# Kernel optimization log

Measured on AMD Instinct MI355X. Metric: run time of the kernel, lower is better.

## Reference

```python
import jax, jax.numpy as jnp
import numpy as np

EMBED_DIM = 1024
NUM_HEADS = 16
SCALE = (EMBED_DIM // NUM_HEADS) ** -0.5  # 0.125


def setup_inputs() -> dict:
    key = jax.random.key(0)
    ks = jax.random.split(key, 9)
    B, S, E = 4, 2048, EMBED_DIM
    std = E ** -0.5
    x = jax.random.normal(ks[0], (B, S, E), dtype=jnp.float32)
    Wq = jax.random.normal(ks[1], (E, E), dtype=jnp.float32) * std
    bq = jax.random.normal(ks[2], (E,), dtype=jnp.float32) * 0.01
    Wk = jax.random.normal(ks[3], (E, E), dtype=jnp.float32) * std
    bk = jax.random.normal(ks[4], (E,), dtype=jnp.float32) * 0.01
    Wv = jax.random.normal(ks[5], (E, E), dtype=jnp.float32) * std
    bv = jax.random.normal(ks[6], (E,), dtype=jnp.float32) * 0.01
    Wo = jax.random.normal(ks[7], (E, E), dtype=jnp.float32) * std
    bo = jax.random.normal(ks[8], (E,), dtype=jnp.float32) * 0.01
    return {"x": x, "Wq": Wq, "bq": bq, "Wk": Wk, "bk": bk,
            "Wv": Wv, "bv": bv, "Wo": Wo, "bo": bo}


def reference(x, Wq, bq, Wk, bk, Wv, bv, Wo, bo):
    # torch nn.Linear: y = x @ W.T + b
    q = jnp.einsum('bse,fe->bsf', x, Wq) + bq   # [B,S,E]
    k = jnp.einsum('bse,fe->bsf', x, Wk) + bk
    v = jnp.einsum('bse,fe->bsf', x, Wv) + bv
    # Bilinear (no softmax) attention: scores = (Q K^T) * scale
    scores = jnp.einsum('bse,bte->bst', q, k) * SCALE  # [B,S,S]
    out = jnp.einsum('bst,bte->bse', scores, v)        # [B,S,E]
    return jnp.einsum('bse,fe->bsf', out, Wo) + bo
```

## Files before the change

kernel.cpp:

```cpp
#include <hip/hip_runtime.h>
#include <stdint.h>

typedef __bf16 bf16_t;
typedef __bf16 bf16x8 __attribute__((ext_vector_type(8)));
typedef __bf16 bf16x4 __attribute__((ext_vector_type(4)));
typedef float floatx4 __attribute__((ext_vector_type(4)));

__device__ __forceinline__ void async_copy16(const bf16_t* g, bf16_t* l) {
  __builtin_amdgcn_global_load_lds(
      (const __attribute__((address_space(1))) void*)g,
      (__attribute__((address_space(3))) void*)l, 16, 0, 0);
}

struct CvtSeg { const float* s; bf16_t* d; long n; };
struct CvtArgs { CvtSeg seg[5]; };

__global__ void cvt_multi(CvtArgs a) {
  CvtSeg sg = a.seg[blockIdx.y];
#pragma unroll
  for (int it = 0; it < 4; it++) {
    long i = (((long)blockIdx.x + (long)it * 2048) * 256 + threadIdx.x) * 4;
    if (i < sg.n) {
      float4 f = *(const float4*)(sg.s + i);
      bf16x4 o;
      o[0] = (bf16_t)f.x; o[1] = (bf16_t)f.y; o[2] = (bf16_t)f.z; o[3] = (bf16_t)f.w;
      *(bf16x4*)(sg.d + i) = o;
    }
  }
}

__global__ __launch_bounds__(256, 2) void qkv3(
    const bf16_t* __restrict__ xb,
    const bf16_t* __restrict__ Wq, const bf16_t* __restrict__ Wk, const bf16_t* __restrict__ Wv,
    const float* __restrict__ bq, const float* __restrict__ bk, const float* __restrict__ bv,
    bf16_t* __restrict__ qout, bf16_t* __restrict__ kT, bf16_t* __restrict__ vT) {
  __shared__ bf16_t As[2 * 4096];
  __shared__ bf16_t Bsh[3][2 * 4096];
  const int L = blockIdx.x;
  const int V = (L & 7) * 64 + (L >> 3);
  const int batch = V >> 7;
  const int rr_   = V & 127;
  const int n0 = (rr_ & 7) * 128;
  const int m0 = (rr_ >> 3) * 128;

  const int tid = threadIdx.x, lane = tid & 63, w = tid >> 6;
  const int wr = w >> 1, wc = w & 1, quad = lane >> 4, lm = lane & 15;
  const int ar = lane >> 2;
  const int ak = (((lane & 3) ^ ((ar >> 1) & 3))) * 8;
  const int swz = (lm >> 1) & 3;

  const bf16_t* ag0 = xb + (long)batch * (2048L * 1024) + (long)(m0 + w * 16 + ar) * 1024 + ak;
  const bf16_t* ag1 = ag0 + 64L * 1024;
  const bf16_t* Wp[3] = {Wq, Wk, Wv};
  const bf16_t* bg0[3];
  const bf16_t* bg1[3];
#pragma unroll
  for (int p = 0; p < 3; p++) {
    bg0[p] = Wp[p] + (long)(n0 + w * 16 + ar) * 1024 + ak;
    bg1[p] = bg0[p] + 64L * 1024;
  }

  floatx4 acc[3][4][4];
#pragma unroll
  for (int p = 0; p < 3; p++)
#pragma unroll
    for (int r = 0; r < 4; r++)
#pragma unroll
      for (int c = 0; c < 4; c++)
        acc[p][r][c] = (floatx4){0.f, 0.f, 0.f, 0.f};

  {
    bf16_t* la = As + w * 512;
    async_copy16(ag0, la);
    async_copy16(ag1, la + 2048);
#pragma unroll
    for (int p = 0; p < 3; p++) {
      bf16_t* lb = Bsh[p] + w * 512;
      async_copy16(bg0[p], lb);
      async_copy16(bg1[p], lb + 2048);
    }
  }
  for (int i = 0; i < 32; i++) {
    __syncthreads();
    if (i + 1 < 32) {
      const int buf = (i + 1) & 1, k0 = (i + 1) * 32;
      bf16_t* la = As + buf * 4096 + w * 512;
      async_copy16(ag0 + k0, la);
      async_copy16(ag1 + k0, la + 2048);
#pragma unroll
      for (int p = 0; p < 3; p++) {
        bf16_t* lb = Bsh[p] + buf * 4096 + w * 512;
        async_copy16(bg0[p] + k0, lb);
        async_copy16(bg1[p] + k0, lb + 2048);
      }
    }
    const bf16_t* Ar = As + (i & 1) * 4096;
    bf16x8 afr[4];
#pragma unroll
    for (int r = 0; r < 4; r++)
      afr[r] = *(const bf16x8*)&Ar[(wr * 64 + r * 16 + lm) * 32 + (quad ^ swz) * 8];
#pragma unroll
    for (int p = 0; p < 3; p++) {
      const bf16_t* Br = Bsh[p] + (i & 1) * 4096;
      bf16x8 bfr[4];
#pragma unroll
      for (int c = 0; c < 4; c++)
        bfr[c] = *(const bf16x8*)&Br[(wc * 64 + c * 16 + lm) * 32 + (quad ^ swz) * 8];
#pragma unroll
      for (int r = 0; r < 4; r++)
#pragma unroll
        for (int c = 0; c < 4; c++)
          acc[p][r][c] = __builtin_amdgcn_mfma_f32_16x16x32_bf16(afr[r], bfr[c], acc[p][r][c], 0, 0, 0);
    }
  }

  const int rowBase = m0 + wr * 64, colBase = n0 + wc * 64;
  {
    bf16_t* C = qout + (long)batch * (2048L * 1024);
#pragma unroll
    for (int r = 0; r < 4; r++) {
      const int row = rowBase + r * 16 + quad * 4;
#pragma unroll
      for (int c = 0; c < 4; c++) {
        const int col = colBase + c * 16 + lm;
        const float bv_ = bq[col];
#pragma unroll
        for (int i = 0; i < 4; i++)
          C[(long)(row + i) * 1024 + col] = (bf16_t)(acc[0][r][c][i] + bv_);
      }
    }
  }
#pragma unroll
  for (int p = 1; p < 3; p++) {
    bf16_t* C = ((p == 1) ? kT : vT) + (long)batch * (1024L * 2048);
    const float* bias = (p == 1) ? bk : bv;
#pragma unroll
    for (int r = 0; r < 4; r++) {
      const int row = rowBase + r * 16 + quad * 4;
#pragma unroll
      for (int c = 0; c < 4; c++) {
        const int col = colBase + c * 16 + lm;
        const float bv_ = bias[col];
        bf16x4 pk;
#pragma unroll
        for (int i = 0; i < 4; i++) pk[i] = (bf16_t)(acc[p][r][c][i] + bv_);
        *(bf16x4*)(C + (long)col * 2048 + row) = pk;
      }
    }
  }
}

template<int OUT_MODE, bool HAS_BIAS, int TOTAL, int BPZ>
__global__ __launch_bounds__(256) void gemm_wp(
    const bf16_t* __restrict__ A, const bf16_t* __restrict__ B,
    void* __restrict__ C, const float* __restrict__ bias,
    int lda, int ldb, int nk, long sA, long sB, long sC, int ldc, float alpha) {
  __shared__ bf16_t Ls[4 * 16384];
  const int L = blockIdx.x;
  const int V = (L & 7) * (TOTAL / 8) + (L >> 3);
  const int batch = V / BPZ;
  const int r_ = V % BPZ;
  const int n0 = (r_ & 7) * 128;
  const int m0 = (r_ >> 3) * 128;

  const int tid = threadIdx.x, lane = tid & 63, w = tid >> 6;
  const int wr = w >> 1, wc = w & 1, quad = lane >> 4, lm = lane & 15;
  const int ar = lane >> 2;
  const int ak = (((lane & 3) ^ ((ar >> 1) & 3))) * 8;
  const int swz = (lm >> 1) & 3;

  bf16_t* Lw = Ls + w * 16384;
  const bf16_t* Ab = A + (long)batch * sA;
  const bf16_t* Bb = B + (long)batch * sB;
  const bf16_t* agA = Ab + (long)(m0 + wr * 64 + ar) * lda + ak;
  const bf16_t* agB = Bb + (long)(n0 + wc * 64 + ar) * ldb + ak;

  auto STAGE = [&](int t, int b) {
    const int k0 = t * 32;
    bf16_t* d = Lw + b * 4096;
#pragma unroll
    for (int j = 0; j < 4; j++)
      async_copy16(agA + (long)j * 16 * lda + k0, d + j * 512);
#pragma unroll
    for (int j = 0; j < 4; j++)
      async_copy16(agB + (long)j * 16 * ldb + k0, d + 2048 + j * 512);
  };

  floatx4 acc[4][4];
#pragma unroll
  for (int r = 0; r < 4; r++)
#pragma unroll
    for (int c = 0; c < 4; c++) acc[r][c] = (floatx4){0.f, 0.f, 0.f, 0.f};

  STAGE(0, 0);
  STAGE(1, 1);
  STAGE(2, 2);
  for (int i = 0; i < nk; i++) {
    const int rem = nk - 1 - i;
    if (rem >= 3) {
      STAGE(i + 3, (i + 3) & 3);
      asm volatile("s_waitcnt vmcnt(24)" ::: "memory");
    } else if (rem == 2) {
      asm volatile("s_waitcnt vmcnt(16)" ::: "memory");
    } else if (rem == 1) {
      asm volatile("s_waitcnt vmcnt(8)" ::: "memory");
    } else {
      asm volatile("s_waitcnt vmcnt(0)" ::: "memory");
    }
    const bf16_t* Aw = Lw + (i & 3) * 4096;
    const bf16_t* Bw = Aw + 2048;
    bf16x8 afr[4], bfr[4];
#pragma unroll
    for (int r = 0; r < 4; r++)
      afr[r] = *(const bf16x8*)&Aw[(r * 16 + lm) * 32 + (quad ^ swz) * 8];
#pragma unroll
    for (int c = 0; c < 4; c++)
      bfr[c] = *(const bf16x8*)&Bw[(c * 16 + lm) * 32 + (quad ^ swz) * 8];
#pragma unroll
    for (int r = 0; r < 4; r++)
#pragma unroll
      for (int c = 0; c < 4; c++)
        acc[r][c] = __builtin_amdgcn_mfma_f32_16x16x32_bf16(afr[r], bfr[c], acc[r][c], 0, 0, 0);
  }

  const int rowBase = m0 + wr * 64, colBase = n0 + wc * 64;
  if (OUT_MODE == 0) {
    bf16_t* Cb = (bf16_t*)C + (long)batch * sC;
#pragma unroll
    for (int r = 0; r < 4; r++) {
      const int row = rowBase + r * 16 + quad * 4;
#pragma unroll
      for (int c = 0; c < 4; c++) {
        const int col = colBase + c * 16 + lm;
        const float bv_ = HAS_BIAS ? bias[col] : 0.f;
#pragma unroll
        for (int i = 0; i < 4; i++)
          Cb[(long)(row + i) * ldc + col] = (bf16_t)(acc[r][c][i] * alpha + bv_);
      }
    }
  } else {
    float* Cf = (float*)C + (long)batch * sC;
#pragma unroll
    for (int r = 0; r < 4; r++) {
      const int row = rowBase + r * 16 + quad * 4;
#pragma unroll
      for (int c = 0; c < 4; c++) {
        const int col = colBase + c * 16 + lm;
        const float bv_ = HAS_BIAS ? bias[col] : 0.f;
#pragma unroll
        for (int i = 0; i < 4; i++)
          Cf[(long)(row + i) * ldc + col] = acc[r][c][i] * alpha + bv_;
      }
    }
  }
}

extern "C" void kernel_launch(void* const* d_in, const int* in_sizes, int n_in,
                              void* d_out, int out_size, void* d_ws, size_t ws_size,
                              hipStream_t stream) {
  const float* x  = (const float*)d_in[0];
  const float* Wq = (const float*)d_in[1];
  const float* bq = (const float*)d_in[2];
  const float* Wk = (const float*)d_in[3];
  const float* bk = (const float*)d_in[4];
  const float* Wv = (const float*)d_in[5];
  const float* bv = (const float*)d_in[6];
  const float* Wo = (const float*)d_in[7];
  const float* bo = (const float*)d_in[8];
  float* out = (float*)d_out;

  const long NX = 8192L * 1024;
  const long NW = 1024L * 1024;

  bf16_t* ws  = (bf16_t*)d_ws;
  bf16_t* xb  = ws;
  bf16_t* Wqb = xb + NX;
  bf16_t* Wkb = Wqb + NW;
  bf16_t* Wvb = Wkb + NW;
  bf16_t* Wob = Wvb + NW;
  bf16_t* qb  = Wob + NW;
  bf16_t* kT  = qb + NX;
  bf16_t* vT  = kT + NX;
  bf16_t* MtTb = xb;
  bf16_t* Gb   = vT;

  CvtArgs ca;
  ca.seg[0] = {x,  xb,  NX};
  ca.seg[1] = {Wq, Wqb, NW};
  ca.seg[2] = {Wk, Wkb, NW};
  ca.seg[3] = {Wv, Wvb, NW};
  ca.seg[4] = {Wo, Wob, NW};
  cvt_multi<<<dim3(2048, 5), 256, 0, stream>>>(ca);

  qkv3<<<dim3(512), 256, 0, stream>>>(xb, Wqb, Wkb, Wvb, bq, bk, bv, qb, kT, vT);

  gemm_wp<0, false, 256, 64><<<dim3(256), 256, 0, stream>>>(
      kT, vT, MtTb, nullptr, 2048, 2048, 64,
      1024L * 2048, 1024L * 2048, 1024L * 1024, 1024, 0.125f);

  gemm_wp<0, false, 256, 64><<<dim3(256), 256, 0, stream>>>(
      Wob, MtTb, Gb, nullptr, 1024, 1024, 32,
      0L, 1024L * 1024, 1024L * 1024, 1024, 1.0f);

  gemm_wp<2, true, 512, 128><<<dim3(512), 256, 0, stream>>>(
      qb, Gb, out, bo, 1024, 1024, 32,
      2048L * 1024, 1024L * 1024, 2048L * 1024, 1024, 1.0f);
}
```

Baseline: 227.3 us.

## Split-K the K^T·V Gram GEMM into two halves and reduce separately

The per-batch K^T·V product (K dimension 2048) now runs as a split-K GEMM over two halves. This doubles the grid from 256 to 512 blocks to fill more CUs, and each half writes a bf16 partial. A new small kernel sums the two halves into the matrix fed to the output-projection GEMM. This adds an extra launch plus partial-buffer write and read traffic, and rounds each partial to bf16 before the sum, which slightly changes precision.

```diff
diff --git a/kernel.cpp b/kernel.cpp
--- a/kernel.cpp
+++ b/kernel.cpp
@@ -27,6 +27,20 @@
       *(bf16x4*)(sg.d + i) = o;
     }
   }
+}
+
+__global__ void cvt_mhalf(const bf16_t* __restrict__ mh, bf16_t* __restrict__ mt) {
+  const long i = ((long)blockIdx.x * 256 + threadIdx.x) * 8;
+  const long b = i >> 20;
+  const long r = i & ((1L << 20) - 1);
+  const bf16_t* h0 = mh + ((b * 2) << 20) + r;
+  const bf16_t* h1 = h0 + (1L << 20);
+  bf16x8 x0 = *(const bf16x8*)h0;
+  bf16x8 x1 = *(const bf16x8*)h1;
+  bf16x8 o;
+#pragma unroll
+  for (int j = 0; j < 8; j++) o[j] = (bf16_t)((float)x0[j] + (float)x1[j]);
+  *(bf16x8*)(mt + i) = o;
 }
 
 __global__ __launch_bounds__(256, 2) void qkv3(
@@ -145,6 +159,106 @@
 #pragma unroll
         for (int i = 0; i < 4; i++) pk[i] = (bf16_t)(acc[p][r][c][i] + bv_);
         *(bf16x4*)(C + (long)col * 2048 + row) = pk;
+      }
+    }
+  }
+}
+
+template<int OUT_MODE, bool HAS_BIAS, int TOTAL, int BPZ, int KSPLIT>
+__global__ __launch_bounds__(256) void gemm_wp2(
+    const bf16_t* __restrict__ A, const bf16_t* __restrict__ B,
+    void* __restrict__ C, const float* __restrict__ bias,
+    int lda, int ldb, int nk, long sA, long sB, long sC, int ldc, float alpha) {
+  __shared__ bf16_t Ls[4 * 8192];
+  const int L = blockIdx.x;
+  const int V = (L & 7) * (TOTAL / 8) + (L >> 3);
+  const int zz = V / BPZ;
+  const int r_ = V % BPZ;
+  const int batch = zz / KSPLIT;
+  const long koff = (long)(zz % KSPLIT) * ((long)nk * 32);
+  const int n0 = (r_ & 7) * 128;
+  const int m0 = (r_ >> 3) * 128;
+
+  const int tid = threadIdx.x, lane = tid & 63, w = tid >> 6;
+  const int wr = w >> 1, wc = w & 1, quad = lane >> 4, lm = lane & 15;
+  const int ar = lane >> 2;
+  const int ak = (((lane & 3) ^ ((ar >> 1) & 3))) * 8;
+  const int swz = (lm >> 1) & 3;
+
+  bf16_t* Lw = Ls + w * 8192;
+  const bf16_t* Ab = A + (long)batch * sA + koff;
+  const bf16_t* Bb = B + (long)batch * sB + koff;
+  const bf16_t* agA = Ab + (long)(m0 + wr * 64 + ar) * lda + ak;
+  const bf16_t* agB = Bb + (long)(n0 + wc * 64 + ar) * ldb + ak;
+
+  auto STAGE = [&](int t, int b) {
+    const int k0 = t * 32;
+    bf16_t* d = Lw + b * 4096;
+#pragma unroll
+    for (int j = 0; j < 4; j++)
+      async_copy16(agA + (long)j * 16 * lda + k0, d + j * 512);
+#pragma unroll
+    for (int j = 0; j < 4; j++)
+      async_copy16(agB + (long)j * 16 * ldb + k0, d + 2048 + j * 512);
+  };
+
+  floatx4 acc[4][4];
+#pragma unroll
+  for (int r = 0; r < 4; r++)
+#pragma unroll
+    for (int c = 0; c < 4; c++) acc[r][c] = (floatx4){0.f, 0.f, 0.f, 0.f};
+
+  STAGE(0, 0);
+  for (int i = 0; i < nk; i++) {
+    if (i + 1 < nk) {
+      STAGE(i + 1, (i + 1) & 1);
+      asm volatile("s_waitcnt vmcnt(8)" ::: "memory");
+    } else {
+      asm volatile("s_waitcnt vmcnt(0)" ::: "memory");
+    }
+    const bf16_t* Aw = Lw + (i & 1) * 4096;
+    const bf16_t* Bw = Aw + 2048;
+    bf16x8 afr[4], bfr[4];
+#pragma unroll
+    for (int r = 0; r < 4; r++)
+      afr[r] = *(const bf16x8*)&Aw[(r * 16 + lm) * 32 + (quad ^ swz) * 8];
+#pragma unroll
+    for (int c = 0; c < 4; c++)
+      bfr[c] = *(const bf16x8*)&Bw[(c * 16 + lm) * 32 + (quad ^ swz) * 8];
+#pragma unroll
+    for (int r = 0; r < 4; r++)
+#pragma unroll
+      for (int c = 0; c < 4; c++)
+        acc[r][c] = __builtin_amdgcn_mfma_f32_16x16x32_bf16(afr[r], bfr[c], acc[r][c], 0, 0, 0);
+  }
+
+  const int rowBase = m0 + wr * 64, colBase = n0 + wc * 64;
+  if (OUT_MODE == 0) {
+    bf16_t* Cb = (bf16_t*)C + (long)zz * sC;
+#pragma unroll
+    for (int r = 0; r < 4; r++) {
+      const int row = rowBase + r * 16 + quad * 4;
+#pragma unroll
+      for (int c = 0; c < 4; c++) {
+        const int col = colBase + c * 16 + lm;
+        const float bv_ = HAS_BIAS ? bias[col] : 0.f;
+#pragma unroll
+        for (int i = 0; i < 4; i++)
+          Cb[(long)(row + i) * ldc + col] = (bf16_t)(acc[r][c][i] * alpha + bv_);
+      }
+    }
+  } else {
+    float* Cf = (float*)C + (long)zz * sC;
+#pragma unroll
+    for (int r = 0; r < 4; r++) {
+      const int row = rowBase + r * 16 + quad * 4;
+#pragma unroll
+      for (int c = 0; c < 4; c++) {
+        const int col = colBase + c * 16 + lm;
+        const float bv_ = HAS_BIAS ? bias[col] : 0.f;
+#pragma unroll
+        for (int i = 0; i < 4; i++)
+          Cf[(long)(row + i) * ldc + col] = acc[r][c][i] * alpha + bv_;
       }
     }
   }
@@ -281,7 +395,8 @@
   bf16_t* qb  = Wob + NW;
   bf16_t* kT  = qb + NX;
   bf16_t* vT  = kT + NX;
-  bf16_t* MtTb = xb;
+  bf16_t* Mh   = xb;
+  bf16_t* MtTb = kT;
   bf16_t* Gb   = vT;
 
   CvtArgs ca;
@@ -294,9 +409,11 @@
 
   qkv3<<<dim3(512), 256, 0, stream>>>(xb, Wqb, Wkb, Wvb, bq, bk, bv, qb, kT, vT);
 
-  gemm_wp<0, false, 256, 64><<<dim3(256), 256, 0, stream>>>(
-      kT, vT, MtTb, nullptr, 2048, 2048, 64,
+  gemm_wp2<0, false, 512, 64, 2><<<dim3(512), 256, 0, stream>>>(
+      kT, vT, Mh, nullptr, 2048, 2048, 32,
       1024L * 2048, 1024L * 2048, 1024L * 1024, 1024, 0.125f);
+
+  cvt_mhalf<<<dim3(2048), 256, 0, stream>>>(Mh, MtTb);
 
   gemm_wp<0, false, 256, 64><<<dim3(256), 256, 0, stream>>>(
       Wob, MtTb, Gb, nullptr, 1024, 1024, 32,
```

Result: slower. 235.7 us (+3.7%).
